# Kernel tuning notes

Hardware: AMD Instinct MI355X
Metric: run time of the kernel (lower is better)

## Reference

```python
import jax, jax.numpy as jnp
import numpy as np

B, L, D = 4, 2048, 1024


def setup_inputs() -> dict:
    key = jax.random.key(0)
    ks = jax.random.split(key, 7)
    scale = 1.0 / np.sqrt(D)
    x = jax.random.normal(ks[0], (B, L, D), dtype=jnp.float32)
    wq = jax.random.normal(ks[1], (D, D), dtype=jnp.float32) * scale
    wk = jax.random.normal(ks[2], (D, D), dtype=jnp.float32) * scale
    wv = jax.random.normal(ks[3], (D, D), dtype=jnp.float32) * scale
    bq = jnp.zeros((D,), dtype=jnp.float32)
    bk = jnp.zeros((D,), dtype=jnp.float32)
    bv = jnp.zeros((D,), dtype=jnp.float32)
    # causal decoder mask, shape [B, 1, L, L] as produced by nn.make_causal_mask
    causal = jnp.tril(jnp.ones((L, L), dtype=bool))
    mask = jnp.broadcast_to(causal[None, None, :, :], (B, 1, L, L))
    return {"x": x, "mask": mask, "wq": wq, "bq": bq, "wk": wk, "bk": bk, "wv": wv, "bv": bv}


def reference(x, mask, wq, bq, wk, bk, wv, bv):
    # q/k/v projections (Dense with bias)
    q = x @ wq + bq            # [B, L, D]
    k = x @ wk + bk
    v = x @ wv + bv
    depth = q.shape[-1]
    q = q / jnp.sqrt(jnp.asarray(depth, dtype=q.dtype))
    attn = jnp.einsum('bqd,bkd->bqk', q, k)          # [B, L, L]
    attn = jnp.where(jnp.squeeze(mask), attn, -999999)
    attn = jax.nn.softmax(attn, axis=-1)
    out = attn @ v                                    # [B, L, D]
    return out
```

## Files before the change

### kernel.cpp

```cpp
#include <hip/hip_runtime.h>

typedef __bf16 bf16_t;
typedef __attribute__((ext_vector_type(8))) __bf16 bf16x8;
typedef __attribute__((ext_vector_type(4))) __bf16 bf16x4;
typedef __attribute__((ext_vector_type(4))) float f32x4;

#define B_  4
#define L_  2048
#define D_  1024
#define M_  (B_*L_)
#define N3_ (3*D_)

__device__ __forceinline__ void gload_lds16(const void* g, void* l) {
  __builtin_amdgcn_global_load_lds(
      (__attribute__((address_space(1))) void*)(g),
      (__attribute__((address_space(3))) void*)(l), 16, 0, 0);
}

__device__ __forceinline__ void stage_tile4(const bf16_t* __restrict__ g, int ld, int grow0,
                                            int k0, bf16_t* lds_tile, int tid) {
  const int lane = tid & 63;
  const int csrc = ((lane & 7) ^ (lane >> 3)) << 3;
  const int rsub = tid >> 3;
  bf16_t* l0 = lds_tile + (size_t)((tid >> 6) << 3) * 64;
  const bf16_t* g0 = g + (size_t)(grow0 + rsub) * ld + (k0 + csrc);
  gload_lds16(g0, l0);
  gload_lds16(g0 + (size_t)32 * ld, l0 + 32 * 64);
  gload_lds16(g0 + (size_t)64 * ld, l0 + 64 * 64);
  gload_lds16(g0 + (size_t)96 * ld, l0 + 96 * 64);
}

#define KTILE4(J, AC, AN1, AN2, BCr, BNx, bC, bN)                                 \
  do {                                                                            \
    const int j_ = (J);                                                           \
    _Pragma("unroll")                                                             \
    for (int mi = 0; mi < 2; ++mi) {                                              \
      aM1_[mi][0] = *(const bf16x8*)(AC + abase + (2 + mi) * 1024 + co0);         \
      aM1_[mi][1] = *(const bf16x8*)(AC + abase + (2 + mi) * 1024 + co1);         \
    }                                                                             \
    if (j_ + 2 < NT) stage_tile4(A, lda, r0, (j_ + 2) * 64, AN2, tid);            \
    asm volatile("s_waitcnt lgkmcnt(4)" ::: "memory");                            \
    __builtin_amdgcn_sched_barrier(0);                                            \
    __builtin_amdgcn_s_setprio(1);                                                \
    _Pragma("unroll")                                                             \
    for (int mi = 0; mi < 2; ++mi)                                                \
      _Pragma("unroll")                                                           \
      for (int ni = 0; ni < 4; ++ni) {                                            \
        acc[mi][ni] = __builtin_amdgcn_mfma_f32_16x16x32_bf16(                    \
            bC[ni][0], aM0_[mi][0], acc[mi][ni], 0, 0, 0);                        \
        acc[mi][ni] = __builtin_amdgcn_mfma_f32_16x16x32_bf16(                    \
            bC[ni][1], aM0_[mi][1], acc[mi][ni], 0, 0, 0);                        \
      }                                                                           \
    __builtin_amdgcn_s_setprio(0);                                                \
    if (j_ + 2 < NT) asm volatile("s_waitcnt vmcnt(4)" ::: "memory");             \
    else             asm volatile("s_waitcnt vmcnt(0)" ::: "memory");             \
    asm volatile("s_barrier" ::: "memory");                                       \
    if (j_ + 1 < NT) {                                                            \
      _Pragma("unroll")                                                           \
      for (int mi = 0; mi < 2; ++mi) {                                            \
        aM0_[mi][0] = *(const bf16x8*)(AN1 + abase + mi * 1024 + co0);            \
        aM0_[mi][1] = *(const bf16x8*)(AN1 + abase + mi * 1024 + co1);            \
      }                                                                           \
      _Pragma("unroll")                                                           \
      for (int ni = 0; ni < 4; ++ni) {                                            \
        bN[ni][0] = *(const bf16x8*)(BNx + bbase + ni * 1024 + co0);              \
        bN[ni][1] = *(const bf16x8*)(BNx + bbase + ni * 1024 + co1);              \
      }                                                                           \
      if (j_ + 2 < NT) stage_tile4(Bt, ldb, c0, (j_ + 2) * 64, BCr, tid);         \
      asm volatile("s_waitcnt lgkmcnt(12)" ::: "memory");                         \
    } else {                                                                      \
      asm volatile("s_waitcnt lgkmcnt(0)" ::: "memory");                          \
    }                                                                             \
    __builtin_amdgcn_sched_barrier(0);                                            \
    __builtin_amdgcn_s_setprio(1);                                                \
    _Pragma("unroll")                                                             \
    for (int mi = 0; mi < 2; ++mi)                                                \
      _Pragma("unroll")                                                           \
      for (int ni = 0; ni < 4; ++ni) {                                            \
        acc[2 + mi][ni] = __builtin_amdgcn_mfma_f32_16x16x32_bf16(                \
            bC[ni][0], aM1_[mi][0], acc[2 + mi][ni], 0, 0, 0);                    \
        acc[2 + mi][ni] = __builtin_amdgcn_mfma_f32_16x16x32_bf16(                \
            bC[ni][1], aM1_[mi][1], acc[2 + mi][ni], 0, 0, 0);                    \
      }                                                                           \
    __builtin_amdgcn_s_setprio(0);                                                \
    asm volatile("s_barrier" ::: "memory");                                       \
  } while (0)

template<bool OUT_BF16, bool CAUSAL, bool VARK, bool PROJ>
__global__ __launch_bounds__(256, 2)
void gemm4(const bf16_t* __restrict__ A, int lda, long sA,
           const bf16_t* __restrict__ Bt, int ldb, long sB,
           void* __restrict__ Cv, int ldc, long sC,
           const float* __restrict__ b0, const float* __restrict__ b1,
           const float* __restrict__ b2, int K)
{
  const int gx = gridDim.x;
  const int nwg = gx * gridDim.y;
  const int orig = blockIdx.y * gx + blockIdx.x;
  const int swz = (orig & 7) * (nwg >> 3) + (orig >> 3);
  const int bx = swz % gx, by = swz / gx;
  if (CAUSAL && bx > by) return;

  const int z = blockIdx.z;
  A  += (size_t)z * sA;
  Bt += (size_t)z * sB;

  const int r0 = by * 128, c0 = bx * 128;
  const int kend = VARK ? min(K, r0 + 128) : K;
  const int NT = kend >> 6;

  extern __shared__ __align__(16) bf16_t smem[];
  bf16_t* Ab0 = smem;
  bf16_t* Ab1 = smem + 8192;
  bf16_t* Ab2 = smem + 16384;
  bf16_t* Bb0 = smem + 24576;
  bf16_t* Bb1 = smem + 32768;

  const int tid = threadIdx.x;
  const int wid = tid >> 6, lane = tid & 63;
  const int wm = wid >> 1, wn = wid & 1;
  const int rl = lane & 15, cg = lane >> 4, x0 = lane & 7;
  const int co0 = ((cg ^ x0) << 3);
  const int co1 = (((4 + cg) ^ x0) << 3);
  const int abase = (wm * 64 + rl) * 64;
  const int bbase = (wn * 64 + rl) * 64;

  f32x4 acc[4][4] = {};
  bf16x8 aM0_[2][2], aM1_[2][2];
  bf16x8 bA_[4][2], bB_[4][2];

  stage_tile4(A,  lda, r0, 0,  Ab0, tid);
  stage_tile4(Bt, ldb, c0, 0,  Bb0, tid);
  stage_tile4(A,  lda, r0, 64, Ab1, tid);
  stage_tile4(Bt, ldb, c0, 64, Bb1, tid);
  asm volatile("s_waitcnt vmcnt(8)" ::: "memory");
  asm volatile("s_barrier" ::: "memory");
  #pragma unroll
  for (int mi = 0; mi < 2; ++mi) {
    aM0_[mi][0] = *(const bf16x8*)(Ab0 + abase + mi * 1024 + co0);
    aM0_[mi][1] = *(const bf16x8*)(Ab0 + abase + mi * 1024 + co1);
  }
  #pragma unroll
  for (int ni = 0; ni < 4; ++ni) {
    bA_[ni][0] = *(const bf16x8*)(Bb0 + bbase + ni * 1024 + co0);
    bA_[ni][1] = *(const bf16x8*)(Bb0 + bbase + ni * 1024 + co1);
  }

  bf16_t *A0 = Ab0, *A1 = Ab1, *A2 = Ab2;
  for (int j = 0; j < NT; j += 2) {
    KTILE4(j,     A0, A1, A2, Bb0, Bb1, bA_, bB_);
    KTILE4(j + 1, A1, A2, A0, Bb1, Bb0, bB_, bA_);
    bf16_t* t = A2; A2 = A1; A1 = A0; A0 = t;
  }

  const int ml = lane & 15, ng = cg * 4;
  #pragma unroll
  for (int mi = 0; mi < 4; ++mi) {
    const int r = r0 + wm * 64 + mi * 16 + ml;
    #pragma unroll
    for (int ni = 0; ni < 4; ++ni) {
      const int c = c0 + wn * 64 + ni * 16 + ng;
      f32x4 v = acc[mi][ni];
      if (PROJ) {
        const float* bias = (c < D_) ? b0 : (c < 2 * D_) ? b1 : b2;
        const float4 bb = *(const float4*)(bias + (c & (D_ - 1)));
        const float sc = (c < D_) ? 0.03125f : 1.0f;
        v[0] = (v[0] + bb.x) * sc; v[1] = (v[1] + bb.y) * sc;
        v[2] = (v[2] + bb.z) * sc; v[3] = (v[3] + bb.w) * sc;
      }
      if (OUT_BF16) {
        bf16x4 o = {(bf16_t)v[0], (bf16_t)v[1], (bf16_t)v[2], (bf16_t)v[3]};
        *(bf16x4*)((bf16_t*)Cv + (size_t)z * sC + (size_t)r * ldc + c) = o;
      } else {
        *(f32x4*)((float*)Cv + (size_t)z * sC + (size_t)r * ldc + c) = v;
      }
    }
  }
}

__device__ __forceinline__ float blk_red_max(float v, float* red, int lane, int wid) {
  #pragma unroll
  for (int o = 32; o; o >>= 1) v = fmaxf(v, __shfl_down(v, o));
  __syncthreads();
  if (lane == 0) red[wid] = v;
  __syncthreads();
  return fmaxf(fmaxf(red[0], red[1]), fmaxf(red[2], red[3]));
}
__device__ __forceinline__ float blk_red_sum(float v, float* red, int lane, int wid) {
  #pragma unroll
  for (int o = 32; o; o >>= 1) v += __shfl_down(v, o);
  __syncthreads();
  if (lane == 0) red[wid] = v;
  __syncthreads();
  return red[0] + red[1] + red[2] + red[3];
}

__global__ __launch_bounds__(256)
void softmax_causal(const bf16_t* __restrict__ S, bf16_t* __restrict__ P) {
  const int r = blockIdx.x;
  const int n = r + 1;
  const int kend = min(((n + 255) >> 8) << 8, L_);
  const bf16_t* row = S + (size_t)blockIdx.y * L_ * L_ + (size_t)r * L_;
  bf16_t* prow = P + (size_t)blockIdx.y * L_ * L_ + (size_t)r * L_;
  const int tid = threadIdx.x, lane = tid & 63, wid = tid >> 6;
  const int c0 = tid * 8;
  __shared__ float red[4];

  const bf16x8 v8 = *(const bf16x8*)(row + c0);
  float s[8];
  #pragma unroll
  for (int i = 0; i < 8; ++i)
    s[i] = (c0 + i < n) ? (float)v8[i] : -3.402823466e38f;

  float mx = s[0];
  #pragma unroll
  for (int i = 1; i < 8; ++i) mx = fmaxf(mx, s[i]);
  mx = blk_red_max(mx, red, lane, wid);

  float e[8]; float sum = 0.f;
  #pragma unroll
  for (int i = 0; i < 8; ++i) {
    const float v = (c0 + i < n) ? __expf(s[i] - mx) : 0.f;
    e[i] = v; sum += v;
  }
  sum = blk_red_sum(sum, red, lane, wid);
  const float inv = 1.0f / sum;

  if (c0 < kend) {
    bf16x8 o;
    #pragma unroll
    for (int i = 0; i < 8; ++i) o[i] = (bf16_t)(e[i] * inv);
    *(bf16x8*)(prow + c0) = o;
  }
}

__global__ void cvt_f32_bf16(const float* __restrict__ in, bf16_t* __restrict__ out, int n4) {
  const int stride = gridDim.x * blockDim.x;
  for (int i = blockIdx.x * blockDim.x + threadIdx.x; i < n4; i += stride) {
    const float4 v = ((const float4*)in)[i];
    bf16x4 o = { (bf16_t)v.x, (bf16_t)v.y, (bf16_t)v.z, (bf16_t)v.w };
    ((bf16x4*)out)[i] = o;
  }
}

__global__ void transpose_w3(const float* __restrict__ w0, const float* __restrict__ w1,
                             const float* __restrict__ w2, bf16_t* __restrict__ oT) {
  const float* w = blockIdx.z == 0 ? w0 : (blockIdx.z == 1 ? w1 : w2);
  bf16_t* o = oT + (size_t)blockIdx.z * D_ * D_;
  __shared__ float t[32][33];
  const int tx = threadIdx.x, ty = threadIdx.y;
  const int x  = blockIdx.x * 32 + tx;
  const int y0 = blockIdx.y * 32;
  #pragma unroll
  for (int j = 0; j < 4; ++j)
    t[ty + j * 8][tx] = w[(size_t)(y0 + ty + j * 8) * D_ + x];
  __syncthreads();
  const int x2 = y0 + tx;
  const int y2 = blockIdx.x * 32;
  #pragma unroll
  for (int j = 0; j < 4; ++j)
    o[(size_t)(y2 + ty + j * 8) * D_ + x2] = (bf16_t)t[tx][ty + j * 8];
}

__global__ void transpose_bf16(const bf16_t* __restrict__ in, int ld_in, int coff,
                               bf16_t* __restrict__ out, int R, int C) {
  __shared__ bf16_t t[32][34];
  const int tx = threadIdx.x, ty = threadIdx.y;
  const int x  = blockIdx.x * 32 + tx;
  const int y0 = blockIdx.y * 32;
  #pragma unroll
  for (int j = 0; j < 4; ++j)
    t[ty + j * 8][tx] = in[(size_t)(y0 + ty + j * 8) * ld_in + coff + x];
  __syncthreads();
  const int x2 = y0 + tx;
  const int y2 = blockIdx.x * 32;
  #pragma unroll
  for (int j = 0; j < 4; ++j)
    out[(size_t)(y2 + ty + j * 8) * R + x2] = t[tx][ty + j * 8];
}

extern "C" void kernel_launch(void* const* d_in, const int* in_sizes, int n_in,
                              void* d_out, int out_size, void* d_ws, size_t ws_size,
                              hipStream_t stream) {
  const float* x  = (const float*)d_in[0];
  const float* wq = (const float*)d_in[2];
  const float* bq = (const float*)d_in[3];
  const float* wk = (const float*)d_in[4];
  const float* bk = (const float*)d_in[5];
  const float* wv = (const float*)d_in[6];
  const float* bv = (const float*)d_in[7];
  float* out = (float*)d_out;

  bf16_t* xb   = (bf16_t*)d_ws;
  bf16_t* wT   = xb  + (size_t)M_ * D_;
  bf16_t* qkv  = wT  + (size_t)N3_ * D_;
  bf16_t* vbT  = qkv + (size_t)M_ * N3_;
  bf16_t* Sb   = vbT + (size_t)M_ * D_;
  bf16_t* Pfull = qkv;

  const size_t SMEM = 81920;

  cvt_f32_bf16<<<1024, 256, 0, stream>>>(x, xb, M_ * D_ / 4);
  transpose_w3<<<dim3(32, 32, 3), dim3(32, 8), 0, stream>>>(wq, wk, wv, wT);

  gemm4<true, false, false, true><<<dim3(N3_ / 128, M_ / 128), 256, SMEM, stream>>>(
      xb, D_, 0, wT, D_, 0, qkv, N3_, 0, bq, bk, bv, D_);

  transpose_bf16<<<dim3(D_ / 32, M_ / 32), dim3(32, 8), 0, stream>>>(qkv, N3_, 2 * D_, vbT, M_, D_);

  gemm4<true, true, false, false><<<dim3(L_ / 128, L_ / 128, B_), 256, SMEM, stream>>>(
      qkv, N3_, (long)L_ * N3_, qkv + D_, N3_, (long)L_ * N3_, Sb, L_, (long)L_ * L_,
      nullptr, nullptr, nullptr, D_);

  softmax_causal<<<dim3(L_, B_), 256, 0, stream>>>(Sb, Pfull);

  gemm4<false, false, true, false><<<dim3(D_ / 128, L_ / 128, B_), 256, SMEM, stream>>>(
      Pfull, L_, (long)L_ * L_, vbT, M_, (long)L_, out, D_, (long)L_ * D_,
      nullptr, nullptr, nullptr, L_);
}
```

Baseline: 168.3 us.

## Load B operand directly from global into registers, dropping B LDS staging

```diff
diff --git a/kernel.cpp b/kernel.cpp
--- a/kernel.cpp
+++ b/kernel.cpp
@@ -30,7 +30,7 @@
   gload_lds16(g0 + (size_t)96 * ld, l0 + 96 * 64);
 }
 
-#define KTILE4(J, AC, AN1, AN2, BCr, BNx, bC, bN)                                 \
+#define KTILE_BD(J, AC, AN1, AN2, bC, bN)                                         \
   do {                                                                            \
     const int j_ = (J);                                                           \
     _Pragma("unroll")                                                             \
@@ -38,8 +38,19 @@
       aM1_[mi][0] = *(const bf16x8*)(AC + abase + (2 + mi) * 1024 + co0);         \
       aM1_[mi][1] = *(const bf16x8*)(AC + abase + (2 + mi) * 1024 + co1);         \
     }                                                                             \
+    if (j_ + 1 < NT) {                                                            \
+      const bf16_t* bp = bbp + (size_t)(j_ + 1) * 64;                             \
+      _Pragma("unroll")                                                           \
+      for (int ni = 0; ni < 4; ++ni) {                                            \
+        bN[ni][0] = *(const bf16x8*)(bp + (size_t)ni * 16 * ldb);                 \
+        bN[ni][1] = *(const bf16x8*)(bp + (size_t)ni * 16 * ldb + 32);            \
+      }                                                                           \
+    }                                                                             \
     if (j_ + 2 < NT) stage_tile4(A, lda, r0, (j_ + 2) * 64, AN2, tid);            \
     asm volatile("s_waitcnt lgkmcnt(4)" ::: "memory");                            \
+    if (j_ + 2 < NT)      asm volatile("s_waitcnt vmcnt(16)" ::: "memory");       \
+    else if (j_ + 1 < NT) asm volatile("s_waitcnt vmcnt(12)" ::: "memory");       \
+    else                  asm volatile("s_waitcnt vmcnt(0)"  ::: "memory");       \
     __builtin_amdgcn_sched_barrier(0);                                            \
     __builtin_amdgcn_s_setprio(1);                                                \
     _Pragma("unroll")                                                             \
@@ -52,8 +63,9 @@
             bC[ni][1], aM0_[mi][1], acc[mi][ni], 0, 0, 0);                        \
       }                                                                           \
     __builtin_amdgcn_s_setprio(0);                                                \
-    if (j_ + 2 < NT) asm volatile("s_waitcnt vmcnt(4)" ::: "memory");             \
-    else             asm volatile("s_waitcnt vmcnt(0)" ::: "memory");             \
+    if (j_ + 2 < NT)      asm volatile("s_waitcnt vmcnt(12)" ::: "memory");       \
+    else if (j_ + 1 < NT) asm volatile("s_waitcnt vmcnt(8)"  ::: "memory");       \
+    else                  asm volatile("s_waitcnt vmcnt(0)"  ::: "memory");       \
     asm volatile("s_barrier" ::: "memory");                                       \
     if (j_ + 1 < NT) {                                                            \
       _Pragma("unroll")                                                           \
@@ -61,13 +73,7 @@
         aM0_[mi][0] = *(const bf16x8*)(AN1 + abase + mi * 1024 + co0);            \
         aM0_[mi][1] = *(const bf16x8*)(AN1 + abase + mi * 1024 + co1);            \
       }                                                                           \
-      _Pragma("unroll")                                                           \
-      for (int ni = 0; ni < 4; ++ni) {                                            \
-        bN[ni][0] = *(const bf16x8*)(BNx + bbase + ni * 1024 + co0);              \
-        bN[ni][1] = *(const bf16x8*)(BNx + bbase + ni * 1024 + co1);              \
-      }                                                                           \
-      if (j_ + 2 < NT) stage_tile4(Bt, ldb, c0, (j_ + 2) * 64, BCr, tid);         \
-      asm volatile("s_waitcnt lgkmcnt(12)" ::: "memory");                         \
+      asm volatile("s_waitcnt lgkmcnt(4)" ::: "memory");                          \
     } else {                                                                      \
       asm volatile("s_waitcnt lgkmcnt(0)" ::: "memory");                          \
     }                                                                             \
@@ -87,13 +93,14 @@
   } while (0)
 
 template<bool OUT_BF16, bool CAUSAL, bool VARK, bool PROJ>
-__global__ __launch_bounds__(256, 2)
+__global__ __launch_bounds__(256, 3)
 void gemm4(const bf16_t* __restrict__ A, int lda, long sA,
-           const bf16_t* __restrict__ Bt, int ldb, long sB,
+           const bf16_t* __restrict__ Bt, int ldb_p, long sB,
            void* __restrict__ Cv, int ldc, long sC,
            const float* __restrict__ b0, const float* __restrict__ b1,
            const float* __restrict__ b2, int K)
 {
+  const int ldb = ldb_p;
   const int gx = gridDim.x;
   const int nwg = gx * gridDim.y;
   const int orig = blockIdx.y * gx + blockIdx.x;
@@ -113,8 +120,6 @@
   bf16_t* Ab0 = smem;
   bf16_t* Ab1 = smem + 8192;
   bf16_t* Ab2 = smem + 16384;
-  bf16_t* Bb0 = smem + 24576;
-  bf16_t* Bb1 = smem + 32768;
 
   const int tid = threadIdx.x;
   const int wid = tid >> 6, lane = tid & 63;
@@ -123,33 +128,31 @@
   const int co0 = ((cg ^ x0) << 3);
   const int co1 = (((4 + cg) ^ x0) << 3);
   const int abase = (wm * 64 + rl) * 64;
-  const int bbase = (wn * 64 + rl) * 64;
+  const bf16_t* bbp = Bt + (size_t)(c0 + wn * 64 + rl) * ldb + cg * 8;
 
   f32x4 acc[4][4] = {};
   bf16x8 aM0_[2][2], aM1_[2][2];
   bf16x8 bA_[4][2], bB_[4][2];
 
-  stage_tile4(A,  lda, r0, 0,  Ab0, tid);
-  stage_tile4(Bt, ldb, c0, 0,  Bb0, tid);
-  stage_tile4(A,  lda, r0, 64, Ab1, tid);
-  stage_tile4(Bt, ldb, c0, 64, Bb1, tid);
-  asm volatile("s_waitcnt vmcnt(8)" ::: "memory");
+  #pragma unroll
+  for (int ni = 0; ni < 4; ++ni) {
+    bA_[ni][0] = *(const bf16x8*)(bbp + (size_t)ni * 16 * ldb);
+    bA_[ni][1] = *(const bf16x8*)(bbp + (size_t)ni * 16 * ldb + 32);
+  }
+  stage_tile4(A, lda, r0, 0,  Ab0, tid);
+  stage_tile4(A, lda, r0, 64, Ab1, tid);
+  asm volatile("s_waitcnt vmcnt(4)" ::: "memory");
   asm volatile("s_barrier" ::: "memory");
   #pragma unroll
   for (int mi = 0; mi < 2; ++mi) {
     aM0_[mi][0] = *(const bf16x8*)(Ab0 + abase + mi * 1024 + co0);
     aM0_[mi][1] = *(const bf16x8*)(Ab0 + abase + mi * 1024 + co1);
   }
-  #pragma unroll
-  for (int ni = 0; ni < 4; ++ni) {
-    bA_[ni][0] = *(const bf16x8*)(Bb0 + bbase + ni * 1024 + co0);
-    bA_[ni][1] = *(const bf16x8*)(Bb0 + bbase + ni * 1024 + co1);
-  }
 
   bf16_t *A0 = Ab0, *A1 = Ab1, *A2 = Ab2;
   for (int j = 0; j < NT; j += 2) {
-    KTILE4(j,     A0, A1, A2, Bb0, Bb1, bA_, bB_);
-    KTILE4(j + 1, A1, A2, A0, Bb1, Bb0, bB_, bA_);
+    KTILE_BD(j,     A0, A1, A2, bA_, bB_);
+    KTILE_BD(j + 1, A1, A2, A0, bB_, bA_);
     bf16_t* t = A2; A2 = A1; A1 = A0; A0 = t;
   }
 
@@ -298,7 +301,7 @@
   bf16_t* Sb   = vbT + (size_t)M_ * D_;
   bf16_t* Pfull = qkv;
 
-  const size_t SMEM = 81920;
+  const size_t SMEM = 49152;
 
   cvt_f32_bf16<<<1024, 256, 0, stream>>>(x, xb, M_ * D_ / 4);
   transpose_w3<<<dim3(32, 32, 3), dim3(32, 8), 0, stream>>>(wq, wk, wv, wT);
```

Measured after the change: 466.3 us. 177% more time.

## Halve GEMM K-tile to 32 to cut LDS and raise occupancy to four blocks

Applied to the files above, without the earlier changes.

```diff
diff --git a/kernel.cpp b/kernel.cpp
--- a/kernel.cpp
+++ b/kernel.cpp
@@ -17,57 +17,43 @@
       (__attribute__((address_space(3))) void*)(l), 16, 0, 0);
 }
 
-__device__ __forceinline__ void stage_tile4(const bf16_t* __restrict__ g, int ld, int grow0,
-                                            int k0, bf16_t* lds_tile, int tid) {
-  const int lane = tid & 63;
-  const int csrc = ((lane & 7) ^ (lane >> 3)) << 3;
-  const int rsub = tid >> 3;
-  bf16_t* l0 = lds_tile + (size_t)((tid >> 6) << 3) * 64;
-  const bf16_t* g0 = g + (size_t)(grow0 + rsub) * ld + (k0 + csrc);
+__device__ __forceinline__ void stage32(const bf16_t* __restrict__ g, int ld, int grow0,
+                                        int k0, bf16_t* lds_tile, int tid) {
+  const int csrc = (((tid & 3) ^ ((tid >> 3) & 3)) << 3);
+  const int row = tid >> 2;
+  bf16_t* l0 = lds_tile + ((tid >> 6) << 9);
+  const bf16_t* g0 = g + (size_t)(grow0 + row) * ld + (k0 + csrc);
   gload_lds16(g0, l0);
-  gload_lds16(g0 + (size_t)32 * ld, l0 + 32 * 64);
-  gload_lds16(g0 + (size_t)64 * ld, l0 + 64 * 64);
-  gload_lds16(g0 + (size_t)96 * ld, l0 + 96 * 64);
-}
-
-#define KTILE4(J, AC, AN1, AN2, BCr, BNx, bC, bN)                                 \
+  gload_lds16(g0 + (size_t)64 * ld, l0 + 2048);
+}
+
+#define KTILE32(J, AC, AN1, AN2, BCr, BNx, bC, bN)                                \
   do {                                                                            \
     const int j_ = (J);                                                           \
-    _Pragma("unroll")                                                             \
-    for (int mi = 0; mi < 2; ++mi) {                                              \
-      aM1_[mi][0] = *(const bf16x8*)(AC + abase + (2 + mi) * 1024 + co0);         \
-      aM1_[mi][1] = *(const bf16x8*)(AC + abase + (2 + mi) * 1024 + co1);         \
-    }                                                                             \
-    if (j_ + 2 < NT) stage_tile4(A, lda, r0, (j_ + 2) * 64, AN2, tid);            \
-    asm volatile("s_waitcnt lgkmcnt(4)" ::: "memory");                            \
+    aM1_[0] = *(const bf16x8*)(AC + abase + 2 * 512 + co);                        \
+    aM1_[1] = *(const bf16x8*)(AC + abase + 3 * 512 + co);                        \
+    if (j_ + 2 < NT) stage32(A, lda, r0, (j_ + 2) * 32, AN2, tid);                \
+    asm volatile("s_waitcnt lgkmcnt(2)" ::: "memory");                            \
     __builtin_amdgcn_sched_barrier(0);                                            \
     __builtin_amdgcn_s_setprio(1);                                                \
     _Pragma("unroll")                                                             \
     for (int mi = 0; mi < 2; ++mi)                                                \
       _Pragma("unroll")                                                           \
-      for (int ni = 0; ni < 4; ++ni) {                                            \
+      for (int ni = 0; ni < 4; ++ni)                                              \
         acc[mi][ni] = __builtin_amdgcn_mfma_f32_16x16x32_bf16(                    \
-            bC[ni][0], aM0_[mi][0], acc[mi][ni], 0, 0, 0);                        \
-        acc[mi][ni] = __builtin_amdgcn_mfma_f32_16x16x32_bf16(                    \
-            bC[ni][1], aM0_[mi][1], acc[mi][ni], 0, 0, 0);                        \
-      }                                                                           \
+            bC[ni], aM0_[mi], acc[mi][ni], 0, 0, 0);                              \
     __builtin_amdgcn_s_setprio(0);                                                \
-    if (j_ + 2 < NT) asm volatile("s_waitcnt vmcnt(4)" ::: "memory");             \
+    if (j_ + 2 < NT) asm volatile("s_waitcnt vmcnt(2)" ::: "memory");             \
     else             asm volatile("s_waitcnt vmcnt(0)" ::: "memory");             \
     asm volatile("s_barrier" ::: "memory");                                       \
     if (j_ + 1 < NT) {                                                            \
+      aM0_[0] = *(const bf16x8*)(AN1 + abase + co);                               \
+      aM0_[1] = *(const bf16x8*)(AN1 + abase + 512 + co);                         \
       _Pragma("unroll")                                                           \
-      for (int mi = 0; mi < 2; ++mi) {                                            \
-        aM0_[mi][0] = *(const bf16x8*)(AN1 + abase + mi * 1024 + co0);            \
-        aM0_[mi][1] = *(const bf16x8*)(AN1 + abase + mi * 1024 + co1);            \
-      }                                                                           \
-      _Pragma("unroll")                                                           \
-      for (int ni = 0; ni < 4; ++ni) {                                            \
-        bN[ni][0] = *(const bf16x8*)(BNx + bbase + ni * 1024 + co0);              \
-        bN[ni][1] = *(const bf16x8*)(BNx + bbase + ni * 1024 + co1);              \
-      }                                                                           \
-      if (j_ + 2 < NT) stage_tile4(Bt, ldb, c0, (j_ + 2) * 64, BCr, tid);         \
-      asm volatile("s_waitcnt lgkmcnt(12)" ::: "memory");                         \
+      for (int ni = 0; ni < 4; ++ni)                                              \
+        bN[ni] = *(const bf16x8*)(BNx + bbase + ni * 512 + co);                   \
+      if (j_ + 2 < NT) stage32(Bt, ldb, c0, (j_ + 2) * 32, BCr, tid);             \
+      asm volatile("s_waitcnt lgkmcnt(6)" ::: "memory");                          \
     } else {                                                                      \
       asm volatile("s_waitcnt lgkmcnt(0)" ::: "memory");                          \
     }                                                                             \
@@ -76,18 +62,15 @@
     _Pragma("unroll")                                                             \
     for (int mi = 0; mi < 2; ++mi)                                                \
       _Pragma("unroll")                                                           \
-      for (int ni = 0; ni < 4; ++ni) {                                            \
+      for (int ni = 0; ni < 4; ++ni)                                              \
         acc[2 + mi][ni] = __builtin_amdgcn_mfma_f32_16x16x32_bf16(                \
-            bC[ni][0], aM1_[mi][0], acc[2 + mi][ni], 0, 0, 0);                    \
-        acc[2 + mi][ni] = __builtin_amdgcn_mfma_f32_16x16x32_bf16(                \
-            bC[ni][1], aM1_[mi][1], acc[2 + mi][ni], 0, 0, 0);                    \
-      }                                                                           \
+            bC[ni], aM1_[mi], acc[2 + mi][ni], 0, 0, 0);                          \
     __builtin_amdgcn_s_setprio(0);                                                \
     asm volatile("s_barrier" ::: "memory");                                       \
   } while (0)
 
 template<bool OUT_BF16, bool CAUSAL, bool VARK, bool PROJ>
-__global__ __launch_bounds__(256, 2)
+__global__ __launch_bounds__(256, 4)
 void gemm4(const bf16_t* __restrict__ A, int lda, long sA,
            const bf16_t* __restrict__ Bt, int ldb, long sB,
            void* __restrict__ Cv, int ldc, long sC,
@@ -107,49 +90,43 @@
 
   const int r0 = by * 128, c0 = bx * 128;
   const int kend = VARK ? min(K, r0 + 128) : K;
-  const int NT = kend >> 6;
+  const int NT = kend >> 5;
 
   extern __shared__ __align__(16) bf16_t smem[];
   bf16_t* Ab0 = smem;
-  bf16_t* Ab1 = smem + 8192;
-  bf16_t* Ab2 = smem + 16384;
-  bf16_t* Bb0 = smem + 24576;
-  bf16_t* Bb1 = smem + 32768;
+  bf16_t* Ab1 = smem + 4096;
+  bf16_t* Ab2 = smem + 8192;
+  bf16_t* Bb0 = smem + 12288;
+  bf16_t* Bb1 = smem + 16384;
 
   const int tid = threadIdx.x;
   const int wid = tid >> 6, lane = tid & 63;
   const int wm = wid >> 1, wn = wid & 1;
-  const int rl = lane & 15, cg = lane >> 4, x0 = lane & 7;
-  const int co0 = ((cg ^ x0) << 3);
-  const int co1 = (((4 + cg) ^ x0) << 3);
-  const int abase = (wm * 64 + rl) * 64;
-  const int bbase = (wn * 64 + rl) * 64;
+  const int rl = lane & 15, cg = lane >> 4;
+  const int co = ((cg ^ ((rl >> 1) & 3)) << 3);
+  const int abase = (wm * 64 + rl) * 32;
+  const int bbase = (wn * 64 + rl) * 32;
 
   f32x4 acc[4][4] = {};
-  bf16x8 aM0_[2][2], aM1_[2][2];
-  bf16x8 bA_[4][2], bB_[4][2];
-
-  stage_tile4(A,  lda, r0, 0,  Ab0, tid);
-  stage_tile4(Bt, ldb, c0, 0,  Bb0, tid);
-  stage_tile4(A,  lda, r0, 64, Ab1, tid);
-  stage_tile4(Bt, ldb, c0, 64, Bb1, tid);
-  asm volatile("s_waitcnt vmcnt(8)" ::: "memory");
+  bf16x8 aM0_[2], aM1_[2];
+  bf16x8 bA_[4], bB_[4];
+
+  stage32(A,  lda, r0, 0,  Ab0, tid);
+  stage32(Bt, ldb, c0, 0,  Bb0, tid);
+  stage32(A,  lda, r0, 32, Ab1, tid);
+  stage32(Bt, ldb, c0, 32, Bb1, tid);
+  asm volatile("s_waitcnt vmcnt(4)" ::: "memory");
   asm volatile("s_barrier" ::: "memory");
-  #pragma unroll
-  for (int mi = 0; mi < 2; ++mi) {
-    aM0_[mi][0] = *(const bf16x8*)(Ab0 + abase + mi * 1024 + co0);
-    aM0_[mi][1] = *(const bf16x8*)(Ab0 + abase + mi * 1024 + co1);
-  }
-  #pragma unroll
-  for (int ni = 0; ni < 4; ++ni) {
-    bA_[ni][0] = *(const bf16x8*)(Bb0 + bbase + ni * 1024 + co0);
-    bA_[ni][1] = *(const bf16x8*)(Bb0 + bbase + ni * 1024 + co1);
-  }
+  aM0_[0] = *(const bf16x8*)(Ab0 + abase + co);
+  aM0_[1] = *(const bf16x8*)(Ab0 + abase + 512 + co);
+  #pragma unroll
+  for (int ni = 0; ni < 4; ++ni)
+    bA_[ni] = *(const bf16x8*)(Bb0 + bbase + ni * 512 + co);
 
   bf16_t *A0 = Ab0, *A1 = Ab1, *A2 = Ab2;
   for (int j = 0; j < NT; j += 2) {
-    KTILE4(j,     A0, A1, A2, Bb0, Bb1, bA_, bB_);
-    KTILE4(j + 1, A1, A2, A0, Bb1, Bb0, bB_, bA_);
+    KTILE32(j,     A0, A1, A2, Bb0, Bb1, bA_, bB_);
+    KTILE32(j + 1, A1, A2, A0, Bb1, Bb0, bB_, bA_);
     bf16_t* t = A2; A2 = A1; A1 = A0; A0 = t;
   }
 
@@ -298,7 +275,7 @@
   bf16_t* Sb   = vbT + (size_t)M_ * D_;
   bf16_t* Pfull = qkv;
 
-  const size_t SMEM = 81920;
+  const size_t SMEM = 40960;
 
   cvt_f32_bf16<<<1024, 256, 0, stream>>>(x, xb, M_ * D_ / 4);
   transpose_w3<<<dim3(32, 32, 3), dim3(32, 8), 0, stream>>>(wq, wk, wv, wT);
```

Result: slower. 381.7 us (+126.7%).
